# Kernel tuning notes

Hardware: AMD Instinct MI355X
Metric: run time of the kernel (lower is better)

The kernel has to match this reference:

```python
import jax, jax.numpy as jnp
import numpy as np

ALPHA = 0.2  # LeakyReLU negative slope
NEG = -9e15


def gat_layer(h, adj, W, a):
    # Faithful to the torch GAT: e_ij = leakyrelu(a^T [Wh_i || Wh_j])
    # = leakyrelu(a_src . Wh_i + a_dst . Wh_j); avoids the NxNx2F materialization.
    Wh = h @ W                              # [N, F]
    Fo = W.shape[1]
    a_src, a_dst = a[:Fo, 0], a[Fo:, 0]
    e = jax.nn.leaky_relu(
        (Wh @ a_src)[:, None] + (Wh @ a_dst)[None, :], negative_slope=ALPHA
    )                                        # [N, N]
    e = jnp.where(adj > 0, e, NEG)
    att = jax.nn.softmax(e, axis=1)          # dropout p=0 (eval)
    return jax.nn.elu(att @ Wh)


def gru_cell(x, h, W_ih, W_hh, b_ih, b_hh):
    # PyTorch GRUCell semantics.
    gi = x @ W_ih.T + b_ih                   # [N, 3F]
    gh = h @ W_hh.T + b_hh
    i_r, i_z, i_n = jnp.split(gi, 3, axis=1)
    h_r, h_z, h_n = jnp.split(gh, 3, axis=1)
    r = jax.nn.sigmoid(i_r + h_r)
    z = jax.nn.sigmoid(i_z + h_z)
    n = jnp.tanh(i_n + r * h_n)
    return (1.0 - z) * n + z * h


def setup_inputs() -> dict:
    key = jax.random.key(0)
    ks = jax.random.split(key, 10)
    N, nfeat, nhid, nout = 8192, 256, 128, 128
    x = jax.random.normal(ks[0], (N, nfeat), dtype=jnp.float32)
    # sparse random binary adjacency (~32 avg degree) + self loops
    adj = (jax.random.uniform(ks[1], (N, N)) < 0.004).astype(jnp.float32)
    adj = jnp.maximum(adj, jnp.eye(N, dtype=jnp.float32))
    h_prev = jnp.zeros((N, nout), dtype=jnp.float32)

    def xavier(k, shape, gain=1.414):
        fan_in, fan_out = shape[0], shape[1]
        b = gain * np.sqrt(6.0 / (fan_in + fan_out))
        return jax.random.uniform(k, shape, jnp.float32, -b, b)

    W1 = xavier(ks[2], (nfeat, nhid))
    a1 = xavier(ks[3], (2 * nhid, 1))
    W2 = xavier(ks[4], (nhid, nout))
    a2 = xavier(ks[5], (2 * nout, 1))
    s = 1.0 / np.sqrt(nout)
    W_ih = jax.random.uniform(ks[6], (3 * nout, nout), jnp.float32, -s, s)
    W_hh = jax.random.uniform(ks[7], (3 * nout, nout), jnp.float32, -s, s)
    b_ih = jax.random.uniform(ks[8], (3 * nout,), jnp.float32, -s, s)
    b_hh = jax.random.uniform(ks[9], (3 * nout,), jnp.float32, -s, s)
    return {"x": x, "adj": adj, "h_prev": h_prev, "W1": W1, "a1": a1,
            "W2": W2, "a2": a2, "W_ih": W_ih, "W_hh": W_hh,
            "b_ih": b_ih, "b_hh": b_hh}


def reference(x, adj, h_prev, W1, a1, W2, a2, W_ih, W_hh, b_ih, b_hh):
    x1 = gat_layer(x, adj, W1, a1)
    h_spat = gat_layer(x1, adj, W2, a2)
    return gru_cell(h_spat, h_prev, W_ih, W_hh, b_ih, b_hh)
```

## Files before the change

### kernel.cpp

```cpp
#include <hip/hip_runtime.h>
#include <math.h>

#define N_NODES 8192
#define CAP 128
#define LRELU_ALPHA 0.2f

typedef float v4f __attribute__((ext_vector_type(4)));

template <int K>
__device__ __forceinline__ void gemm_from_lds(
    int r0, int t, const float* As, const float* __restrict__ W,
    const float* __restrict__ a, float* __restrict__ Wh, float* __restrict__ src,
    float* __restrict__ dst, float (*red)[4][2]) {
  int c = t & 127, half = t >> 7;
  float acc[4] = {0.f, 0.f, 0.f, 0.f};
  const float* Asl = As + (half * 4) * K;
#pragma unroll 8
  for (int k = 0; k < K; k++) {
    float wv = W[k * 128 + c];
#pragma unroll
    for (int r = 0; r < 4; r++) acc[r] += Asl[r * K + k] * wv;
  }
  float as = a[c], ad = a[128 + c];
  int wv_id = t >> 6, lane = t & 63;
#pragma unroll
  for (int r = 0; r < 4; r++) {
    int row = half * 4 + r;
    Wh[(size_t)(r0 + row) * 128 + c] = acc[r];
    float s = acc[r] * as, d = acc[r] * ad;
#pragma unroll
    for (int off = 32; off; off >>= 1) {
      s += __shfl_xor(s, off);
      d += __shfl_xor(d, off);
    }
    if (lane == 0) { red[wv_id][r][0] = s; red[wv_id][r][1] = d; }
  }
  __syncthreads();
  if (t < 8) {
    int wa = (t < 4) ? 0 : 2, rr = t & 3;
    src[r0 + t] = red[wa][rr][0] + red[wa + 1][rr][0];
    dst[r0 + t] = red[wa][rr][1] + red[wa + 1][rr][1];
  }
}

__device__ __forceinline__ float2 agg_node_wave(
    int i, int lane, const float* __restrict__ Wh, const float* __restrict__ src,
    const float* __restrict__ dst, const int* __restrict__ idxbuf,
    const int* __restrict__ counts) {
  int c = counts[i];
  float si = src[i];
  int j0 = 0, j1 = 0;
  float e0 = -1e30f, e1 = -1e30f;
  if (lane < c) {
    j0 = idxbuf[(size_t)i * CAP + lane];
    float xv = si + dst[j0];
    e0 = xv > 0.f ? xv : LRELU_ALPHA * xv;
  }
  if (lane + 64 < c) {
    j1 = idxbuf[(size_t)i * CAP + lane + 64];
    float xv = si + dst[j1];
    e1 = xv > 0.f ? xv : LRELU_ALPHA * xv;
  }
  float m = fmaxf(e0, e1);
#pragma unroll
  for (int off = 32; off; off >>= 1) m = fmaxf(m, __shfl_xor(m, off));
  float w0 = (lane < c) ? expf(e0 - m) : 0.f;
  float w1 = (lane + 64 < c) ? expf(e1 - m) : 0.f;
  float s = w0 + w1;
#pragma unroll
  for (int off = 32; off; off >>= 1) s += __shfl_xor(s, off);
  float inv = 1.f / s;
  const float2* Wh2 = (const float2*)Wh;
  float ax = 0.f, ay = 0.f;
  int cc = c < 64 ? c : 64;
  int k = 0;
  for (; k + 3 < cc; k += 4) {
    float wa = __shfl(w0, k),     wb = __shfl(w0, k + 1);
    float wc_ = __shfl(w0, k + 2), wd = __shfl(w0, k + 3);
    int ja = __shfl(j0, k),     jb = __shfl(j0, k + 1);
    int jc = __shfl(j0, k + 2), jd = __shfl(j0, k + 3);
    float2 va = Wh2[ja * 64 + lane];
    float2 vb = Wh2[jb * 64 + lane];
    float2 vc = Wh2[jc * 64 + lane];
    float2 vd = Wh2[jd * 64 + lane];
    ax += wa * va.x + wb * vb.x + wc_ * vc.x + wd * vd.x;
    ay += wa * va.y + wb * vb.y + wc_ * vc.y + wd * vd.y;
  }
  for (; k < cc; k++) {
    float wk = __shfl(w0, k);
    int jk = __shfl(j0, k);
    float2 v = Wh2[jk * 64 + lane];
    ax += wk * v.x; ay += wk * v.y;
  }
  for (k = 64; k < c; k++) {
    float wk = __shfl(w1, k - 64);
    int jk = __shfl(j1, k - 64);
    float2 v = Wh2[jk * 64 + lane];
    ax += wk * v.x; ay += wk * v.y;
  }
  ax *= inv; ay *= inv;
  return make_float2(ax > 0.f ? ax : expf(ax) - 1.f,
                     ay > 0.f ? ay : expf(ay) - 1.f);
}

__global__ __launch_bounds__(256) void kA(
    const float* __restrict__ adj, int* __restrict__ idxbuf, int* __restrict__ counts,
    const float* __restrict__ x, const float* __restrict__ W1, const float* __restrict__ a1,
    float* __restrict__ Wh1, float* __restrict__ src1, float* __restrict__ dst1,
    const float* __restrict__ Wi, const float* __restrict__ Whm, float* __restrict__ WiT,
    float* __restrict__ WhT) {
  __shared__ float As[8 * 256];
  __shared__ float red[4][4][2];
  __shared__ int jn[CAP];
  __shared__ int cnt;
  int t = threadIdx.x, b = blockIdx.x;
  if (b < N_NODES) {
    if (t == 0) cnt = 0;
    __syncthreads();
    const v4f* row = (const v4f*)(adj + (size_t)b * N_NODES);
    v4f v[8];
#pragma unroll
    for (int u = 0; u < 8; u++) v[u] = __builtin_nontemporal_load(row + t + 256 * u);
#pragma unroll
    for (int u = 0; u < 8; u++) {
      int n = (v[u].x > 0.f) + (v[u].y > 0.f) + (v[u].z > 0.f) + (v[u].w > 0.f);
      if (n) {
        int p = atomicAdd(&cnt, n);
        int j0 = (t + 256 * u) * 4;
        if (v[u].x > 0.f) { if (p < CAP) jn[p] = j0;     p++; }
        if (v[u].y > 0.f) { if (p < CAP) jn[p] = j0 + 1; p++; }
        if (v[u].z > 0.f) { if (p < CAP) jn[p] = j0 + 2; p++; }
        if (v[u].w > 0.f) { if (p < CAP) jn[p] = j0 + 3; p++; }
      }
    }
    __syncthreads();
    int c = cnt > CAP ? CAP : cnt;
    if (t < c) idxbuf[(size_t)b * CAP + t] = jn[t];
    if (t == 0) counts[b] = c;
  } else if (b < N_NODES + 1024) {
    int tile = b - N_NODES;
    const float4* Ab4 = (const float4*)(x + (size_t)tile * 8 * 256);
    float4* As4 = (float4*)As;
#pragma unroll
    for (int l = t; l < 8 * 256 / 4; l += 256) As4[l] = Ab4[l];
    __syncthreads();
    gemm_from_lds<256>(tile * 8, t, As, W1, a1, Wh1, src1, dst1, red);
  } else {
    for (int n = (b - N_NODES - 1024) * 256 + t; n < 384 * 128; n += 64 * 256) {
      int r = n >> 7, c = n & 127;
      WiT[c * 384 + r] = Wi[n];
      WhT[c * 384 + r] = Whm[n];
    }
  }
}

__global__ __launch_bounds__(256) void kB(
    const float* __restrict__ Wh1, const float* __restrict__ src1,
    const float* __restrict__ dst1, const int* __restrict__ idxbuf,
    const int* __restrict__ counts, const float* __restrict__ W2, const float* __restrict__ a2,
    float* __restrict__ Wh2, float* __restrict__ src2, float* __restrict__ dst2) {
  __shared__ float tile[8 * 128];
  __shared__ float red[4][4][2];
  int t = threadIdx.x, b = blockIdx.x;
  int i0 = b * 8;
  int wv = t >> 6, lane = t & 63;
  float2 r0 = agg_node_wave(i0 + wv, lane, Wh1, src1, dst1, idxbuf, counts);
  *(float2*)&tile[wv * 128 + 2 * lane] = r0;
  float2 r1 = agg_node_wave(i0 + 4 + wv, lane, Wh1, src1, dst1, idxbuf, counts);
  *(float2*)&tile[(4 + wv) * 128 + 2 * lane] = r1;
  __syncthreads();
  gemm_from_lds<128>(i0, t, tile, W2, a2, Wh2, src2, dst2, red);
}

__global__ __launch_bounds__(256) void kC(
    const float* __restrict__ Wh2, const float* __restrict__ src2,
    const float* __restrict__ dst2, const int* __restrict__ idxbuf,
    const int* __restrict__ counts, const float* __restrict__ hprev,
    const float* __restrict__ WiT, const float* __restrict__ WhT,
    const float* __restrict__ b_ih, const float* __restrict__ b_hh, float* __restrict__ outp) {
  __shared__ float tile[8 * 128];
  __shared__ float hs[8 * 128];
  int t = threadIdx.x, b = blockIdx.x;
  int i0 = b * 8;
  ((float4*)hs)[t] = ((const float4*)(hprev + (size_t)i0 * 128))[t];
  int wv = t >> 6, lane = t & 63;
  float2 r0 = agg_node_wave(i0 + wv, lane, Wh2, src2, dst2, idxbuf, counts);
  *(float2*)&tile[wv * 128 + 2 * lane] = r0;
  float2 r1 = agg_node_wave(i0 + 4 + wv, lane, Wh2, src2, dst2, idxbuf, counts);
  *(float2*)&tile[(4 + wv) * 128 + 2 * lane] = r1;
  __syncthreads();
  int c = t & 127, half = t >> 7;
  const float* xsl = tile + half * 4 * 128;
  const float* hsl = hs + half * 4 * 128;
  float rg[4], zg[4];
  {
    float ai[4] = {0.f}, ah[4] = {0.f};
#pragma unroll 4
    for (int k = 0; k < 128; k++) {
      float wi = WiT[k * 384 + c], wh = WhT[k * 384 + c];
#pragma unroll
      for (int r = 0; r < 4; r++) { ai[r] += xsl[r * 128 + k] * wi; ah[r] += hsl[r * 128 + k] * wh; }
    }
    float bi = b_ih[c], bh = b_hh[c];
#pragma unroll
    for (int r = 0; r < 4; r++) rg[r] = 1.f / (1.f + expf(-(ai[r] + bi + ah[r] + bh)));
  }
  {
    float ai[4] = {0.f}, ah[4] = {0.f};
#pragma unroll 4
    for (int k = 0; k < 128; k++) {
      float wi = WiT[k * 384 + 128 + c], wh = WhT[k * 384 + 128 + c];
#pragma unroll
      for (int r = 0; r < 4; r++) { ai[r] += xsl[r * 128 + k] * wi; ah[r] += hsl[r * 128 + k] * wh; }
    }
    float bi = b_ih[128 + c], bh = b_hh[128 + c];
#pragma unroll
    for (int r = 0; r < 4; r++) zg[r] = 1.f / (1.f + expf(-(ai[r] + bi + ah[r] + bh)));
  }
  {
    float ai[4] = {0.f}, ah[4] = {0.f};
#pragma unroll 4
    for (int k = 0; k < 128; k++) {
      float wi = WiT[k * 384 + 256 + c], wh = WhT[k * 384 + 256 + c];
#pragma unroll
      for (int r = 0; r < 4; r++) { ai[r] += xsl[r * 128 + k] * wi; ah[r] += hsl[r * 128 + k] * wh; }
    }
    float bi = b_ih[256 + c], bh = b_hh[256 + c];
#pragma unroll
    for (int r = 0; r < 4; r++) {
      float n = tanhf(ai[r] + bi + rg[r] * (ah[r] + bh));
      outp[(size_t)(i0 + half * 4 + r) * 128 + c] =
          (1.f - zg[r]) * n + zg[r] * hsl[r * 128 + c];
    }
  }
}

extern "C" void kernel_launch(void* const* d_in, const int* in_sizes, int n_in,
                              void* d_out, int out_size, void* d_ws, size_t ws_size,
                              hipStream_t stream) {
  const float* x     = (const float*)d_in[0];
  const float* adj   = (const float*)d_in[1];
  const float* hprev = (const float*)d_in[2];
  const float* W1    = (const float*)d_in[3];
  const float* a1    = (const float*)d_in[4];
  const float* W2    = (const float*)d_in[5];
  const float* a2    = (const float*)d_in[6];
  const float* Wi    = (const float*)d_in[7];
  const float* Whm   = (const float*)d_in[8];
  const float* b_ih  = (const float*)d_in[9];
  const float* b_hh  = (const float*)d_in[10];
  float* outp = (float*)d_out;

  char* p = (char*)d_ws;
  float* Wh1    = (float*)p; p += (size_t)N_NODES * 128 * 4;
  float* Wh2    = (float*)p; p += (size_t)N_NODES * 128 * 4;
  float* src1   = (float*)p; p += (size_t)N_NODES * 4;
  float* dst1   = (float*)p; p += (size_t)N_NODES * 4;
  float* src2   = (float*)p; p += (size_t)N_NODES * 4;
  float* dst2   = (float*)p; p += (size_t)N_NODES * 4;
  float* WiT    = (float*)p; p += (size_t)384 * 128 * 4;
  float* WhT    = (float*)p; p += (size_t)384 * 128 * 4;
  int*   counts = (int*)p;   p += (size_t)N_NODES * 4;
  int*   idxbuf = (int*)p;   p += (size_t)N_NODES * CAP * 4;

  kA<<<N_NODES + 1024 + 64, 256, 0, stream>>>(adj, idxbuf, counts, x, W1, a1, Wh1, src1, dst1,
                                              Wi, Whm, WiT, WhT);
  kB<<<N_NODES / 8, 256, 0, stream>>>(Wh1, src1, dst1, idxbuf, counts, W2, a2, Wh2, src2, dst2);
  kC<<<N_NODES / 8, 256, 0, stream>>>(Wh2, src2, dst2, idxbuf, counts, hprev, WiT, WhT, b_ih,
                                      b_hh, outp);
}
```

Measured before the change: 448.6 us.

## Fuse the three GAT/GRU stages into one cooperative kernel with grid syncs

Replaces the three-kernel launch sequence with a single cooperative persistent kernel of 1024 blocks. Each block transposes GRU weights (first 64 blocks), computes the first projection for its 8 rows, then builds neighbor lists for those 8 adjacency rows. It then synchronises the grid before layer-2 aggregation and again before the GRU stage. This removes inter-kernel launch gaps and tails, at the cost of serialising adjacency row scans per block and adding grid-wide barriers. The old path remains as a fallback if the cooperative launch fails.

```diff
diff --git a/kernel.cpp b/kernel.cpp
--- a/kernel.cpp
+++ b/kernel.cpp
@@ -1,9 +1,13 @@
 #include <hip/hip_runtime.h>
+#include <hip/hip_cooperative_groups.h>
 #include <math.h>
+
+namespace cg = cooperative_groups;
 
 #define N_NODES 8192
 #define CAP 128
 #define LRELU_ALPHA 0.2f
+#define NBLK 1024
 
 typedef float v4f __attribute__((ext_vector_type(4)));
 
@@ -103,6 +107,145 @@
                      ay > 0.f ? ay : expf(ay) - 1.f);
 }
 
+__device__ __forceinline__ void gru_tile(
+    int i0, int t, const float* tile, const float* hs, const float* __restrict__ WiT,
+    const float* __restrict__ WhT, const float* __restrict__ b_ih,
+    const float* __restrict__ b_hh, float* __restrict__ outp) {
+  int c = t & 127, half = t >> 7;
+  const float* xsl = tile + half * 4 * 128;
+  const float* hsl = hs + half * 4 * 128;
+  float rg[4], zg[4];
+  {
+    float ai[4] = {0.f}, ah[4] = {0.f};
+#pragma unroll 4
+    for (int k = 0; k < 128; k++) {
+      float wi = WiT[k * 384 + c], wh = WhT[k * 384 + c];
+#pragma unroll
+      for (int r = 0; r < 4; r++) { ai[r] += xsl[r * 128 + k] * wi; ah[r] += hsl[r * 128 + k] * wh; }
+    }
+    float bi = b_ih[c], bh = b_hh[c];
+#pragma unroll
+    for (int r = 0; r < 4; r++) rg[r] = 1.f / (1.f + expf(-(ai[r] + bi + ah[r] + bh)));
+  }
+  {
+    float ai[4] = {0.f}, ah[4] = {0.f};
+#pragma unroll 4
+    for (int k = 0; k < 128; k++) {
+      float wi = WiT[k * 384 + 128 + c], wh = WhT[k * 384 + 128 + c];
+#pragma unroll
+      for (int r = 0; r < 4; r++) { ai[r] += xsl[r * 128 + k] * wi; ah[r] += hsl[r * 128 + k] * wh; }
+    }
+    float bi = b_ih[128 + c], bh = b_hh[128 + c];
+#pragma unroll
+    for (int r = 0; r < 4; r++) zg[r] = 1.f / (1.f + expf(-(ai[r] + bi + ah[r] + bh)));
+  }
+  {
+    float ai[4] = {0.f}, ah[4] = {0.f};
+#pragma unroll 4
+    for (int k = 0; k < 128; k++) {
+      float wi = WiT[k * 384 + 256 + c], wh = WhT[k * 384 + 256 + c];
+#pragma unroll
+      for (int r = 0; r < 4; r++) { ai[r] += xsl[r * 128 + k] * wi; ah[r] += hsl[r * 128 + k] * wh; }
+    }
+    float bi = b_ih[256 + c], bh = b_hh[256 + c];
+#pragma unroll
+    for (int r = 0; r < 4; r++) {
+      float n = tanhf(ai[r] + bi + rg[r] * (ah[r] + bh));
+      outp[(size_t)(i0 + half * 4 + r) * 128 + c] =
+          (1.f - zg[r]) * n + zg[r] * hsl[r * 128 + c];
+    }
+  }
+}
+
+__global__ __launch_bounds__(256, 4) void mega(
+    const float* __restrict__ adj, int* __restrict__ idxbuf, int* __restrict__ counts,
+    const float* __restrict__ x, const float* __restrict__ W1, const float* __restrict__ a1,
+    float* __restrict__ Wh1, float* __restrict__ src1, float* __restrict__ dst1,
+    const float* __restrict__ Wi, const float* __restrict__ Whm, float* __restrict__ WiT,
+    float* __restrict__ WhT, const float* __restrict__ W2, const float* __restrict__ a2,
+    float* __restrict__ Wh2, float* __restrict__ src2, float* __restrict__ dst2,
+    const float* __restrict__ hprev, const float* __restrict__ b_ih,
+    const float* __restrict__ b_hh, float* __restrict__ outp) {
+  __shared__ float As[8 * 256];
+  __shared__ float red[4][4][2];
+  __shared__ int jn[CAP];
+  __shared__ int cnt;
+  int t = threadIdx.x, b = blockIdx.x;
+  cg::grid_group grid = cg::this_grid();
+
+  if (b < 64) {
+    for (int n = b * 256 + t; n < 384 * 128; n += 64 * 256) {
+      int r = n >> 7, c = n & 127;
+      WiT[c * 384 + r] = Wi[n];
+      WhT[c * 384 + r] = Whm[n];
+    }
+  }
+  {
+    const float4* Ab4 = (const float4*)(x + (size_t)b * 8 * 256);
+    float4* As4 = (float4*)As;
+#pragma unroll
+    for (int l = t; l < 8 * 256 / 4; l += 256) As4[l] = Ab4[l];
+    __syncthreads();
+    gemm_from_lds<256>(b * 8, t, As, W1, a1, Wh1, src1, dst1, red);
+  }
+  for (int rr = 0; rr < 8; rr++) {
+    int row = b * 8 + rr;
+    __syncthreads();
+    if (t == 0) cnt = 0;
+    __syncthreads();
+    const v4f* rowp = (const v4f*)(adj + (size_t)row * N_NODES);
+    v4f v[8];
+#pragma unroll
+    for (int u = 0; u < 8; u++) v[u] = __builtin_nontemporal_load(rowp + t + 256 * u);
+#pragma unroll
+    for (int u = 0; u < 8; u++) {
+      int n = (v[u].x > 0.f) + (v[u].y > 0.f) + (v[u].z > 0.f) + (v[u].w > 0.f);
+      if (n) {
+        int p = atomicAdd(&cnt, n);
+        int j0 = (t + 256 * u) * 4;
+        if (v[u].x > 0.f) { if (p < CAP) jn[p] = j0;     p++; }
+        if (v[u].y > 0.f) { if (p < CAP) jn[p] = j0 + 1; p++; }
+        if (v[u].z > 0.f) { if (p < CAP) jn[p] = j0 + 2; p++; }
+        if (v[u].w > 0.f) { if (p < CAP) jn[p] = j0 + 3; p++; }
+      }
+    }
+    __syncthreads();
+    int c = cnt > CAP ? CAP : cnt;
+    if (t < c) idxbuf[(size_t)row * CAP + t] = jn[t];
+    if (t == 0) counts[row] = c;
+  }
+
+  grid.sync();
+
+  {
+    float* tile = As;
+    int wv = t >> 6, lane = t & 63;
+    int i0 = b * 8;
+    float2 r0 = agg_node_wave(i0 + wv, lane, Wh1, src1, dst1, idxbuf, counts);
+    float2 r1 = agg_node_wave(i0 + 4 + wv, lane, Wh1, src1, dst1, idxbuf, counts);
+    *(float2*)&tile[wv * 128 + 2 * lane] = r0;
+    *(float2*)&tile[(4 + wv) * 128 + 2 * lane] = r1;
+    __syncthreads();
+    gemm_from_lds<128>(i0, t, tile, W2, a2, Wh2, src2, dst2, red);
+  }
+
+  grid.sync();
+
+  {
+    float* tile = As;
+    float* hs = As + 8 * 128;
+    ((float4*)hs)[t] = ((const float4*)(hprev + (size_t)b * 8 * 128))[t];
+    int wv = t >> 6, lane = t & 63;
+    int i0 = b * 8;
+    float2 r0 = agg_node_wave(i0 + wv, lane, Wh2, src2, dst2, idxbuf, counts);
+    float2 r1 = agg_node_wave(i0 + 4 + wv, lane, Wh2, src2, dst2, idxbuf, counts);
+    *(float2*)&tile[wv * 128 + 2 * lane] = r0;
+    *(float2*)&tile[(4 + wv) * 128 + 2 * lane] = r1;
+    __syncthreads();
+    gru_tile(i0, t, tile, hs, WiT, WhT, b_ih, b_hh, outp);
+  }
+}
+
 __global__ __launch_bounds__(256) void kA(
     const float* __restrict__ adj, int* __restrict__ idxbuf, int* __restrict__ counts,
     const float* __restrict__ x, const float* __restrict__ W1, const float* __restrict__ a1,
@@ -189,50 +332,7 @@
   float2 r1 = agg_node_wave(i0 + 4 + wv, lane, Wh2, src2, dst2, idxbuf, counts);
   *(float2*)&tile[(4 + wv) * 128 + 2 * lane] = r1;
   __syncthreads();
-  int c = t & 127, half = t >> 7;
-  const float* xsl = tile + half * 4 * 128;
-  const float* hsl = hs + half * 4 * 128;
-  float rg[4], zg[4];
-  {
-    float ai[4] = {0.f}, ah[4] = {0.f};
-#pragma unroll 4
-    for (int k = 0; k < 128; k++) {
-      float wi = WiT[k * 384 + c], wh = WhT[k * 384 + c];
-#pragma unroll
-      for (int r = 0; r < 4; r++) { ai[r] += xsl[r * 128 + k] * wi; ah[r] += hsl[r * 128 + k] * wh; }
-    }
-    float bi = b_ih[c], bh = b_hh[c];
-#pragma unroll
-    for (int r = 0; r < 4; r++) rg[r] = 1.f / (1.f + expf(-(ai[r] + bi + ah[r] + bh)));
-  }
-  {
-    float ai[4] = {0.f}, ah[4] = {0.f};
-#pragma unroll 4
-    for (int k = 0; k < 128; k++) {
-      float wi = WiT[k * 384 + 128 + c], wh = WhT[k * 384 + 128 + c];
-#pragma unroll
-      for (int r = 0; r < 4; r++) { ai[r] += xsl[r * 128 + k] * wi; ah[r] += hsl[r * 128 + k] * wh; }
-    }
-    float bi = b_ih[128 + c], bh = b_hh[128 + c];
-#pragma unroll
-    for (int r = 0; r < 4; r++) zg[r] = 1.f / (1.f + expf(-(ai[r] + bi + ah[r] + bh)));
-  }
-  {
-    float ai[4] = {0.f}, ah[4] = {0.f};
-#pragma unroll 4
-    for (int k = 0; k < 128; k++) {
-      float wi = WiT[k * 384 + 256 + c], wh = WhT[k * 384 + 256 + c];
-#pragma unroll
-      for (int r = 0; r < 4; r++) { ai[r] += xsl[r * 128 + k] * wi; ah[r] += hsl[r * 128 + k] * wh; }
-    }
-    float bi = b_ih[256 + c], bh = b_hh[256 + c];
-#pragma unroll
-    for (int r = 0; r < 4; r++) {
-      float n = tanhf(ai[r] + bi + rg[r] * (ah[r] + bh));
-      outp[(size_t)(i0 + half * 4 + r) * 128 + c] =
-          (1.f - zg[r]) * n + zg[r] * hsl[r * 128 + c];
-    }
-  }
+  gru_tile(i0, t, tile, hs, WiT, WhT, b_ih, b_hh, outp);
 }
 
 extern "C" void kernel_launch(void* const* d_in, const int* in_sizes, int n_in,
@@ -263,9 +363,17 @@
   int*   counts = (int*)p;   p += (size_t)N_NODES * 4;
   int*   idxbuf = (int*)p;   p += (size_t)N_NODES * CAP * 4;
 
-  kA<<<N_NODES + 1024 + 64, 256, 0, stream>>>(adj, idxbuf, counts, x, W1, a1, Wh1, src1, dst1,
-                                              Wi, Whm, WiT, WhT);
-  kB<<<N_NODES / 8, 256, 0, stream>>>(Wh1, src1, dst1, idxbuf, counts, W2, a2, Wh2, src2, dst2);
-  kC<<<N_NODES / 8, 256, 0, stream>>>(Wh2, src2, dst2, idxbuf, counts, hprev, WiT, WhT, b_ih,
-                                      b_hh, outp);
-}
+  void* kargs[] = {
+      (void*)&adj, (void*)&idxbuf, (void*)&counts, (void*)&x, (void*)&W1, (void*)&a1,
+      (void*)&Wh1, (void*)&src1, (void*)&dst1, (void*)&Wi, (void*)&Whm, (void*)&WiT,
+      (void*)&WhT, (void*)&W2, (void*)&a2, (void*)&Wh2, (void*)&src2, (void*)&dst2,
+      (void*)&hprev, (void*)&b_ih, (void*)&b_hh, (void*)&outp};
+  hipError_t e = hipLaunchCooperativeKernel((void*)mega, dim3(NBLK), dim3(256), kargs, 0, stream);
+  if (e != hipSuccess) {
+    kA<<<N_NODES + 1024 + 64, 256, 0, stream>>>(adj, idxbuf, counts, x, W1, a1, Wh1, src1, dst1,
+                                                Wi, Whm, WiT, WhT);
+    kB<<<N_NODES / 8, 256, 0, stream>>>(Wh1, src1, dst1, idxbuf, counts, W2, a2, Wh2, src2, dst2);
+    kC<<<N_NODES / 8, 256, 0, stream>>>(Wh2, src2, dst2, idxbuf, counts, hprev, WiT, WhT, b_ih,
+                                        b_hh, outp);
+  }
+}
```

Result: slower. 714.5 us (+59.3%).
